# Performance work log

Measured on AMD Instinct MI355X. Metric: run time of the kernel, lower is better.

## Reference

```python
import jax, jax.numpy as jnp
import numpy as np

B, S, EH, DH, A = 32, 2048, 512, 512, 512

def setup_inputs() -> dict:
    key = jax.random.key(0)
    k1, k2, k3, k4, k5 = jax.random.split(key, 5)
    decoder_hidden = jax.random.normal(k1, (2, B, DH), dtype=jnp.float32)
    encoder_outputs = jax.random.normal(k2, (B, S, 2 * EH), dtype=jnp.float32)
    # Linear weights stored as (in, out) for x @ W convention
    W = jax.random.normal(k3, (2 * EH, A), dtype=jnp.float32) / np.sqrt(2 * EH)
    U = jax.random.normal(k4, (2 * DH, A), dtype=jnp.float32) / np.sqrt(2 * DH)
    v = jax.random.normal(k5, (A, 1), dtype=jnp.float32) / np.sqrt(A)
    return {"decoder_hidden": decoder_hidden, "encoder_outputs": encoder_outputs,
            "W": W, "U": U, "v": v}

def reference(decoder_hidden, encoder_outputs, W, U, v):
    # (2, B, DH) -> (B, 2*DH), matching transpose(0,1).reshape(B, -1)
    b = decoder_hidden.shape[1]
    dh = jnp.transpose(decoder_hidden, (1, 0, 2)).reshape(b, -1)
    temp1 = jnp.einsum('bse,ea->bsa', encoder_outputs, W)   # (B, S, A)
    temp2 = dh @ U                                          # (B, A) — computed once, broadcast over S
    score = jnp.squeeze(jnp.tanh(temp1 + temp2[:, None, :]) @ v, -1)  # (B, S)
    attention_weights = jax.nn.softmax(score, axis=-1)      # (B, S)
    context_vector = jnp.einsum('bs,bse->be', attention_weights, encoder_outputs)[:, None, :]  # (B,1,2EH)
    return context_vector, attention_weights
```

## Files before the change

kernel.cpp:

```cpp
#include <hip/hip_runtime.h>
#include <hip/hip_bf16.h>

#define Bb 32
#define Ss 2048
#define Kk 1024
#define Aa 512

#define BM 64
#define BK 32
#define NT (Kk / BK)
#define ABUF (BM * BK * 4)

typedef __bf16 bf16x8 __attribute__((ext_vector_type(8)));
typedef float f32x4 __attribute__((ext_vector_type(4)));
typedef float f32x8 __attribute__((ext_vector_type(8)));

__device__ __forceinline__ unsigned short f2bf(float f) {
  unsigned u = __float_as_uint(f);
  u += 0x7FFFu + ((u >> 16) & 1u);
  return (unsigned short)(u >> 16);
}

__device__ __forceinline__ float tanh_fast(float x) {
  float e = __expf(2.f * x);
  return (e - 1.f) / (e + 1.f);
}

__device__ __forceinline__ void gll16(const void* g, void* l) {
  __builtin_amdgcn_global_load_lds(
      (const __attribute__((address_space(1))) unsigned int*)g,
      (__attribute__((address_space(3))) unsigned int*)l, 16, 0, 0);
}

__global__ __launch_bounds__(256) void prep_wt(const float* __restrict__ W,
                                               unsigned short* __restrict__ WtT) {
  const int idx = blockIdx.x * 256 + threadIdx.x;
  const int a = idx & 511;
  const int o = idx >> 9;
  const int t = o >> 2, g = o & 3;
  const int k0 = o * 8;
  unsigned short u[8];
#pragma unroll
  for (int j = 0; j < 8; ++j) u[j] = f2bf(W[(size_t)(k0 + j) * Aa + a]);
  uint4 pk;
  pk.x = (unsigned)u[0] | ((unsigned)u[1] << 16);
  pk.y = (unsigned)u[2] | ((unsigned)u[3] << 16);
  pk.z = (unsigned)u[4] | ((unsigned)u[5] << 16);
  pk.w = (unsigned)u[6] | ((unsigned)u[7] << 16);
  *(uint4*)((char*)WtT + (size_t)t * 32768 + g * 8192 + a * 16) = pk;
}

__global__ __launch_bounds__(256) void t2_partial(const float* __restrict__ dh,
                                                  const float* __restrict__ U,
                                                  float* __restrict__ part) {
  const int b = blockIdx.x, kc = blockIdx.y, t = threadIdx.x;
  __shared__ float sdh[128];
  if (t < 128) {
    int k = kc * 128 + t;
    sdh[t] = dh[(k >> 9) * (Bb * 512) + b * 512 + (k & 511)];
  }
  __syncthreads();
#pragma unroll
  for (int h = 0; h < 2; ++h) {
    const int a = h * 256 + t;
    float s = 0.f;
#pragma unroll 8
    for (int kk = 0; kk < 128; ++kk) s += sdh[kk] * U[(size_t)(kc * 128 + kk) * Aa + a];
    part[(size_t)(b * 8 + kc) * Aa + a] = s;
  }
}

__global__ __launch_bounds__(256) void t2_reduce(const float* __restrict__ part,
                                                 float* __restrict__ t2) {
  const int idx = blockIdx.x * 256 + threadIdx.x;
  const int b = idx >> 9, a = idx & 511;
  float s = 0.f;
#pragma unroll
  for (int kc = 0; kc < 8; ++kc) s += part[(size_t)(b * 8 + kc) * Aa + a];
  t2[idx] = s;
}


#define VM(N)                                                                   \
  asm volatile("s_waitcnt vmcnt(" #N ")" ::: "memory");                         \
  __builtin_amdgcn_sched_barrier(0);

#define AGLL(DST, TT)                                                           \
  if ((TT) < NT) {                                                              \
    const char* eb_ = encC + (TT) * 128;                                        \
    gll16(eb_ + a_gs0, (DST) + a_ld0);                                          \
    gll16(eb_ + a_gs1, (DST) + a_ld1);                                          \
  }

#define BLOAD(BS, TT)                                                           \
  if ((TT) < NT) {                                                              \
    const char* wb_ = wtB + (size_t)(TT) * 32768 + b_voff;                      \
    _Pragma("unroll")                                                           \
    for (int ni = 0; ni < 8; ++ni)                                              \
      BS[ni] = *(const bf16x8*)(wb_ + ni * 256);                                \
  }

#define ITER(AC, BC, AN2, T, VMN)                                               \
  {                                                                             \
    AGLL(AN2, (T) + 2)                                                          \
    __builtin_amdgcn_sched_barrier(0);     \
    bf16x8 af[4];                                                               \
    _Pragma("unroll")                                                           \
    for (int mi = 0; mi < 4; ++mi) {                                            \
      const int rr = mi * 16 + (lane & 15);                                     \
      const int s0 = (lane >> 4) * 2;                                           \
      f32x4 lo = *(const f32x4*)((AC) + rr * 128 + (((s0) ^ (rr & 7)) << 4));   \
      f32x4 hi = *(const f32x4*)((AC) + rr * 128 + (((s0 + 1) ^ (rr & 7)) << 4)); \
      f32x8 w8 = {lo.x, lo.y, lo.z, lo.w, hi.x, hi.y, hi.z, hi.w};              \
      af[mi] = __builtin_convertvector(w8, bf16x8);                             \
    }                                                                           \
    __builtin_amdgcn_s_setprio(1);                                              \
    _Pragma("unroll")                                                           \
    for (int mi = 0; mi < 4; ++mi)                                              \
      _Pragma("unroll")                                                         \
      for (int ni = 0; ni < 8; ++ni)                                            \
        acc[mi][ni] = __builtin_amdgcn_mfma_f32_16x16x32_bf16(af[mi], BC[ni], acc[mi][ni], 0, 0, 0); \
    __builtin_amdgcn_s_setprio(0);                                              \
    BLOAD(BC, (T) + 2)                                                          \
    VM(VMN);                                                                    \
    __builtin_amdgcn_s_barrier();                                               \
  }

__global__ __launch_bounds__(256) void score_gemm(const float* __restrict__ enc,
                                                  const unsigned short* __restrict__ WtT,
                                                  const float* __restrict__ t2,
                                                  const float* __restrict__ v,
                                                  float* __restrict__ score) {
  __shared__ __align__(16) char lds[3 * ABUF];
  char* sA0 = lds;
  char* sA1 = lds + ABUF;
  char* sA2 = lds + 2 * ABUF;

  const int blk = blockIdx.x;
  const int b = blk >> 5, sc = blk & 31;
  const char* encC = (const char*)(enc + (size_t)(b * Ss + sc * BM) * Kk);
  const char* wtB = (const char*)WtT;

  const int tid = threadIdx.x;
  const int lane = tid & 63;
  const int wx = tid >> 6;

  const int a_c0 = tid, a_c1 = 256 + tid;
  const int a_r0 = a_c0 >> 3, a_r1 = a_c1 >> 3;
  const int a_gs0 = a_r0 * 4096 + ((a_c0 & 7) ^ (a_r0 & 7)) * 16;
  const int a_gs1 = a_r1 * 4096 + ((a_c1 & 7) ^ (a_r1 & 7)) * 16;
  const int a_ld0 = a_c0 * 16;
  const int a_ld1 = a_c1 * 16;

  const int b_voff = (lane >> 4) * 8192 + wx * 2048 + (lane & 15) * 16;

  const f32x4 zero = {0.f, 0.f, 0.f, 0.f};
  f32x4 acc[4][8];
#pragma unroll
  for (int i = 0; i < 4; ++i)
#pragma unroll
    for (int j = 0; j < 8; ++j) acc[i][j] = zero;

  bf16x8 b0[8], b1[8];

  {
    AGLL(sA0, 0)
    __builtin_amdgcn_sched_barrier(0);
    BLOAD(b0, 0)
    __builtin_amdgcn_sched_barrier(0);
    AGLL(sA1, 1)
    __builtin_amdgcn_sched_barrier(0);
    BLOAD(b1, 1)
    VM(10);
    __builtin_amdgcn_s_barrier();
  }

  for (int t = 0; t < 30; t += 6) {
    ITER(sA0, b0, sA2, t + 0, 10)
    ITER(sA1, b1, sA0, t + 1, 10)
    ITER(sA2, b0, sA1, t + 2, 10)
    ITER(sA0, b1, sA2, t + 3, 10)
    ITER(sA1, b0, sA0, t + 4, 10)
    ITER(sA2, b1, sA1, t + 5, 10)
  }
  ITER(sA0, b0, sA2, 30, 0)
  ITER(sA1, b1, sA0, 31, 0)

  float t2v[8], vv[8];
#pragma unroll
  for (int ni = 0; ni < 8; ++ni) {
    int c = wx * 128 + ni * 16 + (lane & 15);
    t2v[ni] = t2[b * Aa + c];
    vv[ni] = v[c];
  }
  float sp[4][4];
#pragma unroll
  for (int mi = 0; mi < 4; ++mi)
#pragma unroll
    for (int j = 0; j < 4; ++j) sp[mi][j] = 0.f;
#pragma unroll
  for (int mi = 0; mi < 4; ++mi)
#pragma unroll
    for (int ni = 0; ni < 8; ++ni)
#pragma unroll
      for (int j = 0; j < 4; ++j) {
        float x = acc[mi][ni][j] + t2v[ni];
        sp[mi][j] += vv[ni] * tanh_fast(x);
      }

  float* sbuf = (float*)lds;
#pragma unroll
  for (int mi = 0; mi < 4; ++mi)
#pragma unroll
    for (int j = 0; j < 4; ++j) {
      float s = sp[mi][j];
      s += __shfl_xor(s, 1);
      s += __shfl_xor(s, 2);
      s += __shfl_xor(s, 4);
      s += __shfl_xor(s, 8);
      if ((lane & 15) == 0) {
        int r = mi * 16 + ((lane >> 4) << 2) + j;
        sbuf[r * 4 + wx] = s;
      }
    }
  __syncthreads();
  if (tid < BM) {
    float s = sbuf[tid * 4] + sbuf[tid * 4 + 1] + sbuf[tid * 4 + 2] + sbuf[tid * 4 + 3];
    score[b * Ss + sc * BM + tid] = s;
  }
}

__global__ __launch_bounds__(256) void softmax_k(float* __restrict__ aw) {
  const int b = blockIdx.x, t = threadIdx.x;
  __shared__ float red[8];
  float s[8];
  float m = -3.4e38f;
#pragma unroll
  for (int i = 0; i < 8; ++i) {
    s[i] = aw[b * Ss + t + i * 256];
    m = fmaxf(m, s[i]);
  }
#pragma unroll
  for (int off = 1; off < 64; off <<= 1) m = fmaxf(m, __shfl_xor(m, off));
  const int lane = t & 63, wv = t >> 6;
  if (lane == 0) red[wv] = m;
  __syncthreads();
  m = fmaxf(fmaxf(red[0], red[1]), fmaxf(red[2], red[3]));
  float e[8];
  float l = 0.f;
#pragma unroll
  for (int i = 0; i < 8; ++i) { e[i] = __expf(s[i] - m); l += e[i]; }
#pragma unroll
  for (int off = 1; off < 64; off <<= 1) l += __shfl_xor(l, off);
  if (lane == 0) red[4 + wv] = l;
  __syncthreads();
  l = red[4] + red[5] + red[6] + red[7];
  const float inv = 1.f / l;
#pragma unroll
  for (int i = 0; i < 8; ++i) aw[b * Ss + t + i * 256] = e[i] * inv;
}

__global__ __launch_bounds__(256) void ctx_partial(const float* __restrict__ enc,
                                                   const float* __restrict__ aw,
                                                   float* __restrict__ part) {
  const int b = blockIdx.x, ch = blockIdx.y, t = threadIdx.x;
  __shared__ float sw[64];
  const int s0 = ch * 64;
  if (t < 64) sw[t] = aw[b * Ss + s0 + t];
  __syncthreads();
  float ax = 0.f, ay = 0.f, az = 0.f, aww = 0.f;
  const float* ebase = enc + (size_t)(b * Ss + s0) * Kk + t * 4;
#pragma unroll 4
  for (int r = 0; r < 64; ++r) {
    const float4 ev = *(const float4*)(ebase + (size_t)r * Kk);
    const float w = sw[r];
    ax += w * ev.x; ay += w * ev.y; az += w * ev.z; aww += w * ev.w;
  }
  float4 o; o.x = ax; o.y = ay; o.z = az; o.w = aww;
  *(float4*)(part + (size_t)(b * 32 + ch) * Kk + t * 4) = o;
}

__global__ __launch_bounds__(256) void ctx_reduce(const float* __restrict__ part,
                                                  float* __restrict__ ctx) {
  const int idx = blockIdx.x * 256 + threadIdx.x;
  const int b = idx >> 10, e = idx & 1023;
  float s = 0.f;
#pragma unroll
  for (int ch = 0; ch < 32; ++ch) s += part[(size_t)(b * 32 + ch) * Kk + e];
  ctx[idx] = s;
}

extern "C" void kernel_launch(void* const* d_in, const int* in_sizes, int n_in,
                              void* d_out, int out_size, void* d_ws, size_t ws_size,
                              hipStream_t stream) {
  const float* dh  = (const float*)d_in[0];
  const float* enc = (const float*)d_in[1];
  const float* W   = (const float*)d_in[2];
  const float* U   = (const float*)d_in[3];
  const float* v   = (const float*)d_in[4];

  float* out_ctx = (float*)d_out;
  float* out_aw  = (float*)d_out + 32768;

  char* ws = (char*)d_ws;
  unsigned short* WtT = (unsigned short*)ws;
  float* t2p   = (float*)(ws + 1048576);
  float* t2    = (float*)(ws + 1048576 + 524288);
  float* cpart = (float*)(ws + 1048576 + 524288 + 65536);

  prep_wt<<<256, 256, 0, stream>>>(W, WtT);
  t2_partial<<<dim3(32, 8), 256, 0, stream>>>(dh, U, t2p);
  t2_reduce<<<64, 256, 0, stream>>>(t2p, t2);
  score_gemm<<<1024, 256, 0, stream>>>(enc, WtT, t2, v, out_aw);
  softmax_k<<<32, 256, 0, stream>>>(out_aw);
  ctx_partial<<<dim3(32, 32), 256, 0, stream>>>(enc, out_aw, cpart);
  ctx_reduce<<<128, 256, 0, stream>>>(cpart, out_ctx);
}
```

Baseline: 200.9 us.

## Split score GEMM N dimension across blocks, stage bf16 A and B in LDS

The score GEMM now covers half of the attention dimension per block (BN=256), doubling the grid to 2048 blocks. Each block writes a partial score per slice, and softmax sums the two partials. The A tile is loaded into registers, converted to bf16 once and written to LDS, while the W tile is staged into LDS via global_load_lds instead of per-wave register loads. The aim is higher occupancy (launch bounds 3) and lower register pressure, at the cost of reading the encoder tile twice from global memory and adding a partial-score buffer.

Measured after the change: 179.8 us. 10.5% less time.

```diff
diff --git a/kernel.cpp b/kernel.cpp
--- a/kernel.cpp
+++ b/kernel.cpp
@@ -7,9 +7,11 @@
 #define Aa 512
 
 #define BM 64
+#define BN 256
 #define BK 32
 #define NT (Kk / BK)
-#define ABUF (BM * BK * 4)
+#define ABUF (BM * BK * 2)
+#define BBUF (BN * BK * 2)
 
 typedef __bf16 bf16x8 __attribute__((ext_vector_type(8)));
 typedef float f32x4 __attribute__((ext_vector_type(4)));
@@ -35,10 +37,12 @@
 __global__ __launch_bounds__(256) void prep_wt(const float* __restrict__ W,
                                                unsigned short* __restrict__ WtT) {
   const int idx = blockIdx.x * 256 + threadIdx.x;
-  const int a = idx & 511;
-  const int o = idx >> 9;
-  const int t = o >> 2, g = o & 3;
-  const int k0 = o * 8;
+  const int col = idx & 255;
+  const int q = (idx >> 8) & 3;
+  const int sl = (idx >> 10) & 1;
+  const int t = idx >> 11;
+  const int k0 = t * 32 + q * 8;
+  const int a = sl * 256 + col;
   unsigned short u[8];
 #pragma unroll
   for (int j = 0; j < 8; ++j) u[j] = f2bf(W[(size_t)(k0 + j) * Aa + a]);
@@ -47,7 +51,7 @@
   pk.y = (unsigned)u[2] | ((unsigned)u[3] << 16);
   pk.z = (unsigned)u[4] | ((unsigned)u[5] << 16);
   pk.w = (unsigned)u[6] | ((unsigned)u[7] << 16);
-  *(uint4*)((char*)WtT + (size_t)t * 32768 + g * 8192 + a * 16) = pk;
+  *(uint4*)((char*)WtT + (size_t)((t * 2 + sl) * 1024 + q * 256 + col) * 16) = pk;
 }
 
 __global__ __launch_bounds__(256) void t2_partial(const float* __restrict__ dh,
@@ -85,111 +89,125 @@
   asm volatile("s_waitcnt vmcnt(" #N ")" ::: "memory");                         \
   __builtin_amdgcn_sched_barrier(0);
 
-#define AGLL(DST, TT)                                                           \
+#define ALOAD(S, TT)                                                            \
   if ((TT) < NT) {                                                              \
-    const char* eb_ = encC + (TT) * 128;                                        \
-    gll16(eb_ + a_gs0, (DST) + a_ld0);                                          \
-    gll16(eb_ + a_gs1, (DST) + a_ld1);                                          \
-  }
-
-#define BLOAD(BS, TT)                                                           \
+    const float* ap_ = aG + (TT) * BK;                                          \
+    areg[S][0] = *(const float4*)ap_;                                           \
+    areg[S][1] = *(const float4*)(ap_ + 4);                                     \
+  }
+
+#define AWRITE(DST, S)                                                          \
+  {                                                                             \
+    f32x8 w8_ = {areg[S][0].x, areg[S][0].y, areg[S][0].z, areg[S][0].w,        \
+                 areg[S][1].x, areg[S][1].y, areg[S][1].z, areg[S][1].w};       \
+    *(bf16x8*)((DST) + a_wb) = __builtin_convertvector(w8_, bf16x8);            \
+  }
+
+#define BGLL(TT, DST)                                                           \
   if ((TT) < NT) {                                                              \
-    const char* wb_ = wtB + (size_t)(TT) * 32768 + b_voff;                      \
+    const char* wb_ = wtB + (size_t)((TT) * 2 + slice) * 16384;                 \
+    gll16(wb_ + b_c0, (DST) + b_c0);                                            \
+    gll16(wb_ + b_c1, (DST) + b_c1);                                            \
+    gll16(wb_ + b_c2, (DST) + b_c2);                                            \
+    gll16(wb_ + b_c3, (DST) + b_c3);                                            \
+  }
+
+#define ITER(AC, BC, AN, SL, SW, T, VMN)                                        \
+  {                                                                             \
+    bf16x8 af[4], bfr[4];                                                       \
     _Pragma("unroll")                                                           \
-    for (int ni = 0; ni < 8; ++ni)                                              \
-      BS[ni] = *(const bf16x8*)(wb_ + ni * 256);                                \
-  }
-
-#define ITER(AC, BC, AN2, T, VMN)                                               \
-  {                                                                             \
-    AGLL(AN2, (T) + 2)                                                          \
-    __builtin_amdgcn_sched_barrier(0);     \
-    bf16x8 af[4];                                                               \
+    for (int mi = 0; mi < 4; ++mi)                                              \
+      af[mi] = *(const bf16x8*)((AC) + (lane >> 4) * 1024 +                     \
+                                (mi * 16 + (lane & 15)) * 16);                  \
     _Pragma("unroll")                                                           \
-    for (int mi = 0; mi < 4; ++mi) {                                            \
-      const int rr = mi * 16 + (lane & 15);                                     \
-      const int s0 = (lane >> 4) * 2;                                           \
-      f32x4 lo = *(const f32x4*)((AC) + rr * 128 + (((s0) ^ (rr & 7)) << 4));   \
-      f32x4 hi = *(const f32x4*)((AC) + rr * 128 + (((s0 + 1) ^ (rr & 7)) << 4)); \
-      f32x8 w8 = {lo.x, lo.y, lo.z, lo.w, hi.x, hi.y, hi.z, hi.w};              \
-      af[mi] = __builtin_convertvector(w8, bf16x8);                             \
-    }                                                                           \
+    for (int ni = 0; ni < 4; ++ni)                                              \
+      bfr[ni] = *(const bf16x8*)((BC) + (lane >> 4) * 4096 +                    \
+                                 (wx * 64 + ni * 16 + (lane & 15)) * 16);       \
+    ALOAD(SL, (T) + 2)                                                          \
     __builtin_amdgcn_s_setprio(1);                                              \
     _Pragma("unroll")                                                           \
     for (int mi = 0; mi < 4; ++mi)                                              \
       _Pragma("unroll")                                                         \
-      for (int ni = 0; ni < 8; ++ni)                                            \
-        acc[mi][ni] = __builtin_amdgcn_mfma_f32_16x16x32_bf16(af[mi], BC[ni], acc[mi][ni], 0, 0, 0); \
+      for (int ni = 0; ni < 4; ++ni)                                            \
+        acc[mi][ni] = __builtin_amdgcn_mfma_f32_16x16x32_bf16(af[mi], bfr[ni], acc[mi][ni], 0, 0, 0); \
     __builtin_amdgcn_s_setprio(0);                                              \
-    BLOAD(BC, (T) + 2)                                                          \
-    VM(VMN);                                                                    \
-    __builtin_amdgcn_s_barrier();                                               \
-  }
-
-__global__ __launch_bounds__(256) void score_gemm(const float* __restrict__ enc,
-                                                  const unsigned short* __restrict__ WtT,
-                                                  const float* __restrict__ t2,
-                                                  const float* __restrict__ v,
-                                                  float* __restrict__ score) {
-  __shared__ __align__(16) char lds[3 * ABUF];
+    __builtin_amdgcn_sched_barrier(0);                                          \
+    __builtin_amdgcn_s_barrier();             \
+    BGLL((T) + 2, BC)                                                           \
+    VM(VMN)                                                                     \
+    if ((T) + 1 < NT) { AWRITE(AN, SW) }                                        \
+    asm volatile("s_waitcnt lgkmcnt(0)" ::: "memory");                          \
+    __builtin_amdgcn_sched_barrier(0);                                          \
+    __builtin_amdgcn_s_barrier();                       \
+  }
+
+__global__ __launch_bounds__(256, 3) void score_gemm(const float* __restrict__ enc,
+                                                     const unsigned short* __restrict__ WtT,
+                                                     const float* __restrict__ t2,
+                                                     const float* __restrict__ v,
+                                                     float* __restrict__ psc) {
+  __shared__ __align__(16) char lds[2 * ABUF + 2 * BBUF];
   char* sA0 = lds;
   char* sA1 = lds + ABUF;
-  char* sA2 = lds + 2 * ABUF;
+  char* sB0 = lds + 2 * ABUF;
+  char* sB1 = lds + 2 * ABUF + BBUF;
 
   const int blk = blockIdx.x;
-  const int b = blk >> 5, sc = blk & 31;
-  const char* encC = (const char*)(enc + (size_t)(b * Ss + sc * BM) * Kk);
+  const int mtile = blk >> 1, slice = blk & 1;
+  const int b = mtile >> 5;
+  const float* encF = enc + (size_t)mtile * BM * Kk;
   const char* wtB = (const char*)WtT;
 
   const int tid = threadIdx.x;
   const int lane = tid & 63;
   const int wx = tid >> 6;
 
-  const int a_c0 = tid, a_c1 = 256 + tid;
-  const int a_r0 = a_c0 >> 3, a_r1 = a_c1 >> 3;
-  const int a_gs0 = a_r0 * 4096 + ((a_c0 & 7) ^ (a_r0 & 7)) * 16;
-  const int a_gs1 = a_r1 * 4096 + ((a_c1 & 7) ^ (a_r1 & 7)) * 16;
-  const int a_ld0 = a_c0 * 16;
-  const int a_ld1 = a_c1 * 16;
-
-  const int b_voff = (lane >> 4) * 8192 + wx * 2048 + (lane & 15) * 16;
+  const int a_row = tid >> 2;
+  const int a_q = tid & 3;
+  const float* aG = encF + (size_t)a_row * Kk + a_q * 8;
+  const int a_wb = a_q * 1024 + a_row * 16;
+
+  const int b_c0 = (0 * 256 + tid) * 16;
+  const int b_c1 = (1 * 256 + tid) * 16;
+  const int b_c2 = (2 * 256 + tid) * 16;
+  const int b_c3 = (3 * 256 + tid) * 16;
 
   const f32x4 zero = {0.f, 0.f, 0.f, 0.f};
-  f32x4 acc[4][8];
+  f32x4 acc[4][4];
 #pragma unroll
   for (int i = 0; i < 4; ++i)
 #pragma unroll
-    for (int j = 0; j < 8; ++j) acc[i][j] = zero;
-
-  bf16x8 b0[8], b1[8];
+    for (int j = 0; j < 4; ++j) acc[i][j] = zero;
+
+  float4 areg[2][2];
 
   {
-    AGLL(sA0, 0)
+    ALOAD(0, 0)
     __builtin_amdgcn_sched_barrier(0);
-    BLOAD(b0, 0)
+    BGLL(0, sB0)
     __builtin_amdgcn_sched_barrier(0);
-    AGLL(sA1, 1)
+    ALOAD(1, 1)
     __builtin_amdgcn_sched_barrier(0);
-    BLOAD(b1, 1)
-    VM(10);
+    BGLL(1, sB1)
+    VM(10)
+    AWRITE(sA0, 0)
+    VM(6)
+    asm volatile("s_waitcnt lgkmcnt(0)" ::: "memory");
+    __builtin_amdgcn_sched_barrier(0);
     __builtin_amdgcn_s_barrier();
   }
 
-  for (int t = 0; t < 30; t += 6) {
-    ITER(sA0, b0, sA2, t + 0, 10)
-    ITER(sA1, b1, sA0, t + 1, 10)
-    ITER(sA2, b0, sA1, t + 2, 10)
-    ITER(sA0, b1, sA2, t + 3, 10)
-    ITER(sA1, b0, sA0, t + 4, 10)
-    ITER(sA2, b1, sA1, t + 5, 10)
-  }
-  ITER(sA0, b0, sA2, 30, 0)
-  ITER(sA1, b1, sA0, 31, 0)
-
-  float t2v[8], vv[8];
-#pragma unroll
-  for (int ni = 0; ni < 8; ++ni) {
-    int c = wx * 128 + ni * 16 + (lane & 15);
+  for (int t = 0; t < 30; t += 2) {
+    ITER(sA0, sB0, sA1, 0, 1, t, 6)
+    ITER(sA1, sB1, sA0, 1, 0, t + 1, 6)
+  }
+  ITER(sA0, sB0, sA1, 0, 1, 30, 0)
+  ITER(sA1, sB1, sA0, 1, 0, 31, 0)
+
+  float t2v[4], vv[4];
+#pragma unroll
+  for (int ni = 0; ni < 4; ++ni) {
+    int c = slice * BN + wx * 64 + ni * 16 + (lane & 15);
     t2v[ni] = t2[b * Aa + c];
     vv[ni] = v[c];
   }
@@ -201,7 +219,7 @@
 #pragma unroll
   for (int mi = 0; mi < 4; ++mi)
 #pragma unroll
-    for (int ni = 0; ni < 8; ++ni)
+    for (int ni = 0; ni < 4; ++ni)
 #pragma unroll
       for (int j = 0; j < 4; ++j) {
         float x = acc[mi][ni][j] + t2v[ni];
@@ -226,18 +244,20 @@
   __syncthreads();
   if (tid < BM) {
     float s = sbuf[tid * 4] + sbuf[tid * 4 + 1] + sbuf[tid * 4 + 2] + sbuf[tid * 4 + 3];
-    score[b * Ss + sc * BM + tid] = s;
-  }
-}
-
-__global__ __launch_bounds__(256) void softmax_k(float* __restrict__ aw) {
+    psc[slice * 65536 + mtile * BM + tid] = s;
+  }
+}
+
+__global__ __launch_bounds__(256) void softmax_k(const float* __restrict__ psc,
+                                                 float* __restrict__ aw) {
   const int b = blockIdx.x, t = threadIdx.x;
   __shared__ float red[8];
   float s[8];
   float m = -3.4e38f;
 #pragma unroll
   for (int i = 0; i < 8; ++i) {
-    s[i] = aw[b * Ss + t + i * 256];
+    int idx = b * Ss + t + i * 256;
+    s[i] = psc[idx] + psc[65536 + idx];
     m = fmaxf(m, s[i]);
   }
 #pragma unroll
@@ -307,12 +327,13 @@
   float* t2p   = (float*)(ws + 1048576);
   float* t2    = (float*)(ws + 1048576 + 524288);
   float* cpart = (float*)(ws + 1048576 + 524288 + 65536);
+  float* psc   = (float*)(ws + 1048576 + 524288 + 65536 + 4194304);
 
   prep_wt<<<256, 256, 0, stream>>>(W, WtT);
   t2_partial<<<dim3(32, 8), 256, 0, stream>>>(dh, U, t2p);
   t2_reduce<<<64, 256, 0, stream>>>(t2p, t2);
-  score_gemm<<<1024, 256, 0, stream>>>(enc, WtT, t2, v, out_aw);
-  softmax_k<<<32, 256, 0, stream>>>(out_aw);
+  score_gemm<<<2048, 256, 0, stream>>>(enc, WtT, t2, v, psc);
+  softmax_k<<<32, 256, 0, stream>>>(psc, out_aw);
   ctx_partial<<<dim3(32, 32), 256, 0, stream>>>(enc, out_aw, cpart);
   ctx_reduce<<<128, 256, 0, stream>>>(cpart, out_ctx);
 }
```
